# Kernel optimization log

Measured on AMD Instinct MI355X. Metric: run time of the kernel, lower is better.

The kernel has to match this reference:

```python
import jax, jax.numpy as jnp
import numpy as np

N, K, D, P, B = 16384, 64, 128, 8, 32
LN_EPS = 1e-5


def _silu(x):
    return x * jax.nn.sigmoid(x)


def setup_inputs() -> dict:
    key = jax.random.key(0)
    ks = jax.random.split(key, 12)
    s = 1.0 / np.sqrt(D)
    return {
        "x_scalar": jax.random.normal(ks[0], (N, D), jnp.float32),
        "k_dot_r": jax.random.normal(ks[1], (N, K), jnp.float32) * 3.0,
        "sinc_damping": jax.random.uniform(ks[2], (N, K), jnp.float32),
        "batch": jnp.sort(jax.random.randint(ks[3], (N,), 0, B)),
        "down_projection": jax.random.normal(ks[4], (K, P), jnp.float32),
        "W_pre1": jax.random.normal(ks[5], (D, D), jnp.float32) * s,
        "W_pre2": jax.random.normal(ks[6], (D, D), jnp.float32) * s,
        "ln_gamma": jnp.ones((D,), jnp.float32),
        "ln_beta": jnp.zeros((D,), jnp.float32),
        "W_up": jax.random.normal(ks[7], (D, P), jnp.float32) * (1.0 / np.sqrt(P)) * 0.01,
        "W_upd1": jax.random.normal(ks[8], (D, D), jnp.float32) * s,
        "W_upd2": jax.random.normal(ks[9], (D, D), jnp.float32) * s,
    }


def reference(x_scalar, k_dot_r, sinc_damping, batch, down_projection,
              W_pre1, W_pre2, ln_gamma, ln_beta, W_up, W_upd1, W_upd2):
    # pre_mlp residual: x + act(act(x W1^T) W2^T)
    h = _silu(_silu(x_scalar @ W_pre1.T) @ W_pre2.T)
    x_res = x_scalar + h
    # LayerNorm over feature dim
    mu = jnp.mean(x_res, axis=-1, keepdims=True)
    var = jnp.mean(jnp.square(x_res - mu), axis=-1, keepdims=True)
    x_res = (x_res - mu) * jax.lax.rsqrt(var + LN_EPS) * ln_gamma + ln_beta
    # trig structure factors
    real = jnp.cos(k_dot_r) * sinc_damping  # [N, K]
    imag = jnp.sin(k_dot_r) * sinc_damping  # [N, K]
    # scatter-sum per graph: sf[b,k,d] = sum_{n in b} trig[n,k] * x_res[n,d]
    sf_real = jax.ops.segment_sum(real[:, :, None] * x_res[:, None, :], batch, num_segments=B)
    sf_imag = jax.ops.segment_sum(imag[:, :, None] * x_res[:, None, :], batch, num_segments=B)
    # k-space filter: [K, D]
    kfilter = down_projection @ W_up.T
    # gather back per node and reduce over K
    fr = (kfilter[None, :, :] * sf_real)[batch]  # [N, K, D]
    fi = (kfilter[None, :, :] * sf_imag)[batch]  # [N, K, D]
    ewald_message = jnp.einsum('nkd,nk->nd', fr, real) + jnp.einsum('nkd,nk->nd', fi, imag)
    x = x_scalar + ewald_message
    return x + _silu(_silu(x @ W_upd1.T) @ W_upd2.T)
```

## Files before the change

### kernel.cpp

```cpp
#include <hip/hip_runtime.h>
#include <stdint.h>

#define NN 16384
#define KK 64
#define DD 128
#define PP 8
#define NB 32
#define CH 64
#define CHD 32

typedef unsigned short ushort_t;
typedef __attribute__((ext_vector_type(8))) short short8;
typedef __attribute__((ext_vector_type(4))) float f32x4;

__device__ __forceinline__ ushort_t f2bf(float x) {
    unsigned u = __float_as_uint(x);
    u += 0x7fffu + ((u >> 16) & 1u);
    return (ushort_t)(u >> 16);
}
__device__ __forceinline__ float silu_f(float v) { return v / (1.0f + __expf(-v)); }

__device__ __forceinline__ short8 ldWf(const float* __restrict__ W, int row, int col) {
    float4 a = *(const float4*)&W[(size_t)row * DD + col];
    float4 b = *(const float4*)&W[(size_t)row * DD + col + 4];
    short8 v;
    v[0] = (short)f2bf(a.x); v[1] = (short)f2bf(a.y);
    v[2] = (short)f2bf(a.z); v[3] = (short)f2bf(a.w);
    v[4] = (short)f2bf(b.x); v[5] = (short)f2bf(b.y);
    v[6] = (short)f2bf(b.z); v[7] = (short)f2bf(b.w);
    return v;
}

__global__ __launch_bounds__(256, 4) void kB_pre(
        const float* __restrict__ x, const float* __restrict__ W1,
        const float* __restrict__ W2, const float* __restrict__ W3,
        const float* __restrict__ W4, const float* __restrict__ gamma,
        const float* __restrict__ beta, const float* __restrict__ kdr,
        const float* __restrict__ damp, ushort_t* __restrict__ Wb,
        ushort_t* __restrict__ trig_rm, ushort_t* __restrict__ trigTb,
        ushort_t* __restrict__ xresTb) {
    __shared__ __align__(16) ushort_t xsb[32][136];
    __shared__ __align__(16) ushort_t t1b[32][136];
    __shared__ float2 lnp[32][2];
    const int bid = blockIdx.x;

    if (bid < 8) {
        int w = bid;
        const float* s = ((w >> 2) == 0 ? W3 : W4) + (w & 3) * 4096;
        ushort_t* d = Wb + (size_t)(w >> 2) * 16384 + (w & 3) * 4096;
        for (int i = threadIdx.x; i < 4096; i += 256) d[i] = f2bf(s[i]);
        return;
    }

    const int t = threadIdx.x, lane = t & 63, wv = t >> 6;
    const int ci = bid - 8;
    const int n0 = ci * 32;

    float2 kvp[4], dvp[4];
#pragma unroll
    for (int q = 0; q < 4; ++q) {
        int i = t + q * 256;
        int r = i >> 5, kk = (i & 31) * 2;
        kvp[q] = *(const float2*)&kdr[(size_t)(n0 + r) * KK + kk];
        dvp[q] = *(const float2*)&damp[(size_t)(n0 + r) * KK + kk];
    }
    {
        const float4* src = (const float4*)(x + (size_t)n0 * DD);
        for (int i = t; i < 512; i += 256) {
            float4 v0 = src[i * 2], v1 = src[i * 2 + 1];
            int r = i >> 4, c = (i & 15) << 3;
            short8 pk;
            pk[0] = (short)f2bf(v0.x); pk[1] = (short)f2bf(v0.y);
            pk[2] = (short)f2bf(v0.z); pk[3] = (short)f2bf(v0.w);
            pk[4] = (short)f2bf(v1.x); pk[5] = (short)f2bf(v1.y);
            pk[6] = (short)f2bf(v1.z); pk[7] = (short)f2bf(v1.w);
            *(short8*)&xsb[r][c] = pk;
        }
    }
    __syncthreads();

    const int ar0 = (wv & 1) * 16;
    const int chf = (wv >> 1) * 64;
    const int fr = (lane >> 4) * 8, cr = lane & 15, rr4 = (lane >> 4) * 4;
    f32x4 acc[4];
    const f32x4 z4 = {0.f, 0.f, 0.f, 0.f};

#pragma unroll
    for (int nt = 0; nt < 4; ++nt) acc[nt] = z4;
#pragma unroll
    for (int ks = 0; ks < 4; ++ks) {
        short8 af = *(const short8*)&xsb[ar0 + cr][ks * 32 + fr];
#pragma unroll
        for (int nt = 0; nt < 4; ++nt) {
            short8 bf = ldWf(W1, chf + nt * 16 + cr, ks * 32 + fr);
            acc[nt] = __builtin_amdgcn_mfma_f32_16x16x32_bf16(af, bf, acc[nt], 0, 0, 0);
        }
    }
#pragma unroll
    for (int nt = 0; nt < 4; ++nt)
#pragma unroll
        for (int r = 0; r < 4; ++r)
            t1b[ar0 + rr4 + r][chf + nt * 16 + cr] = f2bf(silu_f(acc[nt][r]));
    __syncthreads();

#pragma unroll
    for (int nt = 0; nt < 4; ++nt) acc[nt] = z4;
#pragma unroll
    for (int ks = 0; ks < 4; ++ks) {
        short8 af = *(const short8*)&t1b[ar0 + cr][ks * 32 + fr];
#pragma unroll
        for (int nt = 0; nt < 4; ++nt) {
            short8 bf = ldWf(W2, chf + nt * 16 + cr, ks * 32 + fr);
            acc[nt] = __builtin_amdgcn_mfma_f32_16x16x32_bf16(af, bf, acc[nt], 0, 0, 0);
        }
    }
#pragma unroll
    for (int q = 0; q < 4; ++q) {
        int i = t + q * 256;
        int r = i >> 5, kk = (i & 31) * 2;
        float s0, c0, s1, c1;
        __sincosf(kvp[q].x, &s0, &c0);
        __sincosf(kvp[q].y, &s1, &c1);
        ushort_t rc0 = f2bf(c0 * dvp[q].x), rc1 = f2bf(c1 * dvp[q].y);
        ushort_t is0 = f2bf(s0 * dvp[q].x), is1 = f2bf(s1 * dvp[q].y);
        xsb[r][kk] = rc0; xsb[r][kk + 1] = rc1;
        xsb[r][64 + kk] = is0; xsb[r][64 + kk + 1] = is1;
        ushort2 a; a.x = rc0; a.y = rc1;
        ushort2 b; b.x = is0; b.y = is1;
        *(ushort2*)&trig_rm[(size_t)(n0 + r) * 128 + kk] = a;
        *(ushort2*)&trig_rm[(size_t)(n0 + r) * 128 + 64 + kk] = b;
    }
    float g[4], be[4];
#pragma unroll
    for (int nt = 0; nt < 4; ++nt) {
        g[nt] = gamma[chf + nt * 16 + cr];
        be[nt] = beta[chf + nt * 16 + cr];
    }
#pragma unroll
    for (int r = 0; r < 4; ++r) {
        int row = n0 + ar0 + rr4 + r;
        float s = 0.f, sq = 0.f;
#pragma unroll
        for (int nt = 0; nt < 4; ++nt) {
            float v = x[(size_t)row * DD + chf + nt * 16 + cr] + silu_f(acc[nt][r]);
            acc[nt][r] = v;
            s += v; sq += v * v;
        }
#pragma unroll
        for (int off = 1; off < 16; off <<= 1) {
            s += __shfl_xor(s, off);
            sq += __shfl_xor(sq, off);
        }
        if (cr == 0) {
            float2 p; p.x = s; p.y = sq;
            lnp[ar0 + rr4 + r][wv >> 1] = p;
        }
    }
    __syncthreads();

#pragma unroll
    for (int r = 0; r < 4; ++r) {
        int row = ar0 + rr4 + r;
        float2 a = lnp[row][0], b = lnp[row][1];
        float s = a.x + b.x, sq = a.y + b.y;
        float mu = s * (1.0f / 128.0f);
        float var = sq * (1.0f / 128.0f) - mu * mu;
        float rs = rsqrtf(var + 1e-5f);
#pragma unroll
        for (int nt = 0; nt < 4; ++nt)
            t1b[row][chf + nt * 16 + cr] = f2bf((acc[nt][r] - mu) * rs * g[nt] + be[nt]);
    }
    __syncthreads();

    {
        int m = t >> 1, hh = (t & 1) * 16;
        size_t base = (size_t)(ci >> 1) * 8192 + (size_t)m * 64 + (ci & 1) * 32 + hh;
#pragma unroll
        for (int q = 0; q < 2; ++q) {
            short8 v;
#pragma unroll
            for (int j = 0; j < 8; ++j) v[j] = (short)xsb[hh + q * 8 + j][m];
            *(short8*)&trigTb[base + q * 8] = v;
        }
#pragma unroll
        for (int q = 0; q < 2; ++q) {
            short8 v;
#pragma unroll
            for (int j = 0; j < 8; ++j) v[j] = (short)t1b[hh + q * 8 + j][m];
            *(short8*)&xresTb[base + q * 8] = v;
        }
    }
}

__global__ __launch_bounds__(256, 4) void kS_scatter(
        const int* __restrict__ batch,
        const ushort_t* __restrict__ xresTb, const ushort_t* __restrict__ trigTb,
        const float* __restrict__ dp, const float* __restrict__ wup,
        ushort_t* __restrict__ SFTb) {
    __shared__ __align__(16) ushort_t xt[16][72];
    __shared__ __align__(16) ushort_t tt[64][72];
    __shared__ int seg2[2];
    const int b = blockIdx.x & 31, g2 = blockIdx.x >> 5;
    const int d0 = (g2 & 7) * 16, mh = (g2 >> 3) * 64;
    const int t = threadIdx.x, lane = t & 63, wv = t >> 6;

    if (t < 2) {
        int tgt = b + t;
        int lo = 0, hi = NN;
        while (lo < hi) { int mid = (lo + hi) >> 1; if (batch[mid] < tgt) lo = mid + 1; else hi = mid; }
        seg2[t] = lo;
    }
    __syncthreads();
    const int segs = seg2[0], sege = seg2[1];

    const int fr = (lane >> 4) * 8, cr = lane & 15, rr4 = (lane >> 4) * 4;
    const f32x4 z4 = {0.f, 0.f, 0.f, 0.f};
    f32x4 acc = z4;

    for (int r0 = segs & ~(CH - 1); r0 < sege; r0 += CH) {
        int lo = segs - r0; if (lo < 0) lo = 0;
        int hi = sege - r0; if (hi > CH) hi = CH;
        const size_t cb = (size_t)(r0 >> 6) * 8192;
        for (int i = t; i < 160; i += 256) {
            int row = i >> 1, h = (i & 1) * 32;
            const ushort_t* src = (row < 16 ? xresTb + cb + (size_t)(d0 + row) * 64
                                            : trigTb + cb + (size_t)(mh + row - 16) * 64) + h;
            ushort_t* dst = (row < 16 ? &xt[row][h] : &tt[row - 16][h]);
            if (lo == 0 && hi == CH) {
#pragma unroll
                for (int q = 0; q < 4; ++q) *(short8*)(dst + q * 8) = *(const short8*)(src + q * 8);
            } else {
                for (int j = 0; j < 32; ++j) { int c = h + j; dst[j] = (c >= lo && c < hi) ? src[j] : (ushort_t)0; }
            }
        }
        __syncthreads();
#pragma unroll
        for (int ks = 0; ks < 2; ++ks) {
            short8 af = *(const short8*)&xt[cr][ks * 32 + fr];
            short8 bf = *(const short8*)&tt[wv * 16 + cr][ks * 32 + fr];
            acc = __builtin_amdgcn_mfma_f32_16x16x32_bf16(af, bf, acc, 0, 0, 0);
        }
        __syncthreads();
    }

    const int m = mh + wv * 16 + cr;
    const int k = m & 63;
    float4 p0 = *(const float4*)&dp[k * PP];
    float4 p1 = *(const float4*)&dp[k * PP + 4];
#pragma unroll
    for (int r = 0; r < 4; ++r) {
        int d = d0 + rr4 + r;
        float4 w0 = *(const float4*)&wup[d * PP];
        float4 w1 = *(const float4*)&wup[d * PP + 4];
        float kf = p0.x * w0.x + p0.y * w0.y + p0.z * w0.z + p0.w * w0.w
                 + p1.x * w1.x + p1.y * w1.y + p1.z * w1.z + p1.w * w1.w;
        SFTb[((size_t)b * 128 + d) * 128 + m] = f2bf(acc[r] * kf);
    }
}

__global__ __launch_bounds__(256, 3) void kD_post(
        const float* __restrict__ x, const int* __restrict__ batch,
        const ushort_t* __restrict__ trig_rm, const ushort_t* __restrict__ SFTb,
        const ushort_t* __restrict__ Wb, float* __restrict__ out) {
    __shared__ __align__(16) ushort_t sft[128 * 136];
    __shared__ __align__(16) ushort_t xs[32][136];
    __shared__ int starts[NB + 1];
    __shared__ int offs[NB + 1];
    const int t = threadIdx.x, lane = t & 63, wv = t >> 6;
    const int fr = (lane >> 4) * 8, cr = lane & 15, rr4 = (lane >> 4) * 4;
    const f32x4 z4 = {0.f, 0.f, 0.f, 0.f};

    if (t < 33) {
        int lo;
        if (t == NB) lo = NN;
        else {
            lo = 0; int hi = NN;
            while (lo < hi) { int mid = (lo + hi) >> 1; if (batch[mid] < t) lo = mid + 1; else hi = mid; }
        }
        starts[t] = lo;
    }
    __syncthreads();
    if (t == 0) {
        int off = 0;
        for (int b = 0; b < NB; ++b) {
            offs[b] = off;
            off += (starts[b + 1] - starts[b] + CHD - 1) / CHD;
        }
        offs[NB] = off;
    }
    __syncthreads();
    const int nwl = offs[NB];
    const int c = (blockIdx.x & 7) * 72 + (blockIdx.x >> 3);
    if (c >= nwl) return;
    int b = 0;
    while (offs[b + 1] <= c) ++b;
    const int r0c = starts[b] + (c - offs[b]) * CHD;
    const int len = min(CHD, starts[b + 1] - r0c);

    const int ar0 = (wv & 1) * 16;
    const int chf = (wv >> 1) * 64;
    const ushort_t* W3b = Wb;
    const ushort_t* W4b = Wb + 16384;

    int nrow = r0c + ar0 + cr; if (nrow >= NN) nrow = NN - 1;
    short8 afp[4];
#pragma unroll
    for (int ks = 0; ks < 4; ++ks)
        afp[ks] = *(const short8*)&trig_rm[(size_t)nrow * 128 + ks * 32 + fr];
    float xr[4][4];
#pragma unroll
    for (int nt = 0; nt < 4; ++nt)
#pragma unroll
        for (int r = 0; r < 4; ++r) {
            int row = r0c + ar0 + rr4 + r; if (row >= NN) row = NN - 1;
            xr[nt][r] = x[(size_t)row * DD + chf + nt * 16 + cr];
        }

    {
        const ushort_t* srcS = SFTb + (size_t)b * 16384;
        for (int i = t; i < 2048; i += 256) {
            int r = i >> 4, cc = (i & 15) * 8;
            *(short8*)&sft[r * 136 + cc] = *(const short8*)(srcS + r * 128 + cc);
        }
    }
    __syncthreads();

    f32x4 g4[4];
#pragma unroll
    for (int nt = 0; nt < 4; ++nt) g4[nt] = z4;
#pragma unroll
    for (int ks = 0; ks < 4; ++ks) {
#pragma unroll
        for (int nt = 0; nt < 4; ++nt) {
            short8 bf = *(const short8*)&sft[(chf + nt * 16 + cr) * 136 + ks * 32 + fr];
            g4[nt] = __builtin_amdgcn_mfma_f32_16x16x32_bf16(afp[ks], bf, g4[nt], 0, 0, 0);
        }
    }

    float xk[4][4];
#pragma unroll
    for (int nt = 0; nt < 4; ++nt)
#pragma unroll
        for (int r = 0; r < 4; ++r) {
            int rr = ar0 + rr4 + r;
            float xv = xr[nt][r] + g4[nt][r];
            xk[nt][r] = xv;
            xs[rr][chf + nt * 16 + cr] = f2bf(xv);
        }
    __syncthreads();

#pragma unroll
    for (int nt = 0; nt < 4; ++nt) g4[nt] = z4;
#pragma unroll
    for (int ks = 0; ks < 4; ++ks) {
        short8 af = *(const short8*)&xs[ar0 + cr][ks * 32 + fr];
#pragma unroll
        for (int nt = 0; nt < 4; ++nt) {
            short8 bf = *(const short8*)&W3b[(size_t)(chf + nt * 16 + cr) * DD + ks * 32 + fr];
            g4[nt] = __builtin_amdgcn_mfma_f32_16x16x32_bf16(af, bf, g4[nt], 0, 0, 0);
        }
    }
#pragma unroll
    for (int nt = 0; nt < 4; ++nt)
#pragma unroll
        for (int r = 0; r < 4; ++r)
            sft[(ar0 + rr4 + r) * 136 + chf + nt * 16 + cr] = f2bf(silu_f(g4[nt][r]));
    __syncthreads();

#pragma unroll
    for (int nt = 0; nt < 4; ++nt) g4[nt] = z4;
#pragma unroll
    for (int ks = 0; ks < 4; ++ks) {
        short8 af = *(const short8*)&sft[(ar0 + cr) * 136 + ks * 32 + fr];
#pragma unroll
        for (int nt = 0; nt < 4; ++nt) {
            short8 bf = *(const short8*)&W4b[(size_t)(chf + nt * 16 + cr) * DD + ks * 32 + fr];
            g4[nt] = __builtin_amdgcn_mfma_f32_16x16x32_bf16(af, bf, g4[nt], 0, 0, 0);
        }
    }
#pragma unroll
    for (int nt = 0; nt < 4; ++nt)
#pragma unroll
        for (int r = 0; r < 4; ++r) {
            int rr = ar0 + rr4 + r;
            if (rr < len)
                out[(size_t)(r0c + rr) * DD + chf + nt * 16 + cr] = xk[nt][r] + silu_f(g4[nt][r]);
        }
}

extern "C" void kernel_launch(void* const* d_in, const int* in_sizes, int n_in,
                              void* d_out, int out_size, void* d_ws, size_t ws_size,
                              hipStream_t stream) {
    const float* x      = (const float*)d_in[0];
    const float* kdr    = (const float*)d_in[1];
    const float* damp   = (const float*)d_in[2];
    const int*   batch  = (const int*)d_in[3];
    const float* dp     = (const float*)d_in[4];
    const float* W_pre1 = (const float*)d_in[5];
    const float* W_pre2 = (const float*)d_in[6];
    const float* gamma  = (const float*)d_in[7];
    const float* beta   = (const float*)d_in[8];
    const float* W_up   = (const float*)d_in[9];
    const float* W_upd1 = (const float*)d_in[10];
    const float* W_upd2 = (const float*)d_in[11];
    float* out = (float*)d_out;

    char* w = (char*)d_ws;
    ushort_t* Wb      = (ushort_t*)w;
    size_t o = 131072;
    ushort_t* trig_rm = (ushort_t*)(w + o);  o += (size_t)NN * 128 * 2;
    ushort_t* trigTb  = (ushort_t*)(w + o);  o += (size_t)NN * 128 * 2;
    ushort_t* xresTb  = (ushort_t*)(w + o);  o += (size_t)NN * 128 * 2;
    ushort_t* SFTb    = (ushort_t*)(w + o);  o += (size_t)NB * 128 * 128 * 2;

    hipLaunchKernelGGL(kB_pre, dim3(8 + NN / 32), dim3(256), 0, stream,
                       x, W_pre1, W_pre2, W_upd1, W_upd2, gamma, beta,
                       kdr, damp, Wb, trig_rm, trigTb, xresTb);
    hipLaunchKernelGGL(kS_scatter, dim3(NB * 16), dim3(256), 0, stream,
                       batch, xresTb, trigTb, dp, W_up, SFTb);
    hipLaunchKernelGGL(kD_post, dim3(576), dim3(256), 0, stream,
                       x, batch, trig_rm, SFTb, Wb, out);
}
```

Before: 67.91 us.

## Halve pre-kernel row tile to 16 and compute segment starts once

The pre-MLP/LayerNorm kernel now handles 16 rows per block instead of 32, so it launches twice as many blocks. Each wave covers a 32-column slice, and the LayerNorm partial sums are reduced over four waves. A dedicated block computes the graph segment starts by binary search once and writes them to workspace, so the scatter and post kernels no longer repeat that search in every block. The cost is that W1/W2 fragments are reloaded from global memory twice as often across blocks, and the transposed output writes become narrower.

```diff
diff --git a/kernel.cpp b/kernel.cpp
--- a/kernel.cpp
+++ b/kernel.cpp
@@ -36,12 +36,13 @@
         const float* __restrict__ W2, const float* __restrict__ W3,
         const float* __restrict__ W4, const float* __restrict__ gamma,
         const float* __restrict__ beta, const float* __restrict__ kdr,
-        const float* __restrict__ damp, ushort_t* __restrict__ Wb,
+        const float* __restrict__ damp, const int* __restrict__ batch,
+        ushort_t* __restrict__ Wb, int* __restrict__ starts_g,
         ushort_t* __restrict__ trig_rm, ushort_t* __restrict__ trigTb,
         ushort_t* __restrict__ xresTb) {
-    __shared__ __align__(16) ushort_t xsb[32][136];
-    __shared__ __align__(16) ushort_t t1b[32][136];
-    __shared__ float2 lnp[32][2];
+    __shared__ __align__(16) ushort_t xsb[16][136];
+    __shared__ __align__(16) ushort_t t1b[16][136];
+    __shared__ float2 lnp[16][4];
     const int bid = blockIdx.x;
 
     if (bid < 8) {
@@ -51,14 +52,27 @@
         for (int i = threadIdx.x; i < 4096; i += 256) d[i] = f2bf(s[i]);
         return;
     }
+    if (bid == 8) {
+        const int t = threadIdx.x;
+        if (t <= NB) {
+            int lo;
+            if (t == NB) lo = NN;
+            else {
+                lo = 0; int hi = NN;
+                while (lo < hi) { int mid = (lo + hi) >> 1; if (batch[mid] < t) lo = mid + 1; else hi = mid; }
+            }
+            starts_g[t] = lo;
+        }
+        return;
+    }
 
     const int t = threadIdx.x, lane = t & 63, wv = t >> 6;
-    const int ci = bid - 8;
-    const int n0 = ci * 32;
-
-    float2 kvp[4], dvp[4];
-#pragma unroll
-    for (int q = 0; q < 4; ++q) {
+    const int ci = bid - 9;
+    const int n0 = ci * 16;
+
+    float2 kvp[2], dvp[2];
+#pragma unroll
+    for (int q = 0; q < 2; ++q) {
         int i = t + q * 256;
         int r = i >> 5, kk = (i & 31) * 2;
         kvp[q] = *(const float2*)&kdr[(size_t)(n0 + r) * KK + kk];
@@ -66,56 +80,53 @@
     }
     {
         const float4* src = (const float4*)(x + (size_t)n0 * DD);
-        for (int i = t; i < 512; i += 256) {
-            float4 v0 = src[i * 2], v1 = src[i * 2 + 1];
-            int r = i >> 4, c = (i & 15) << 3;
-            short8 pk;
-            pk[0] = (short)f2bf(v0.x); pk[1] = (short)f2bf(v0.y);
-            pk[2] = (short)f2bf(v0.z); pk[3] = (short)f2bf(v0.w);
-            pk[4] = (short)f2bf(v1.x); pk[5] = (short)f2bf(v1.y);
-            pk[6] = (short)f2bf(v1.z); pk[7] = (short)f2bf(v1.w);
-            *(short8*)&xsb[r][c] = pk;
-        }
-    }
-    __syncthreads();
-
-    const int ar0 = (wv & 1) * 16;
-    const int chf = (wv >> 1) * 64;
+        float4 v0 = src[t * 2], v1 = src[t * 2 + 1];
+        int r = t >> 4, c = (t & 15) << 3;
+        short8 pk;
+        pk[0] = (short)f2bf(v0.x); pk[1] = (short)f2bf(v0.y);
+        pk[2] = (short)f2bf(v0.z); pk[3] = (short)f2bf(v0.w);
+        pk[4] = (short)f2bf(v1.x); pk[5] = (short)f2bf(v1.y);
+        pk[6] = (short)f2bf(v1.z); pk[7] = (short)f2bf(v1.w);
+        *(short8*)&xsb[r][c] = pk;
+    }
+    __syncthreads();
+
+    const int chf = wv * 32;
     const int fr = (lane >> 4) * 8, cr = lane & 15, rr4 = (lane >> 4) * 4;
-    f32x4 acc[4];
+    f32x4 acc[2];
     const f32x4 z4 = {0.f, 0.f, 0.f, 0.f};
 
 #pragma unroll
-    for (int nt = 0; nt < 4; ++nt) acc[nt] = z4;
+    for (int nt = 0; nt < 2; ++nt) acc[nt] = z4;
 #pragma unroll
     for (int ks = 0; ks < 4; ++ks) {
-        short8 af = *(const short8*)&xsb[ar0 + cr][ks * 32 + fr];
-#pragma unroll
-        for (int nt = 0; nt < 4; ++nt) {
+        short8 af = *(const short8*)&xsb[cr][ks * 32 + fr];
+#pragma unroll
+        for (int nt = 0; nt < 2; ++nt) {
             short8 bf = ldWf(W1, chf + nt * 16 + cr, ks * 32 + fr);
             acc[nt] = __builtin_amdgcn_mfma_f32_16x16x32_bf16(af, bf, acc[nt], 0, 0, 0);
         }
     }
 #pragma unroll
-    for (int nt = 0; nt < 4; ++nt)
+    for (int nt = 0; nt < 2; ++nt)
 #pragma unroll
         for (int r = 0; r < 4; ++r)
-            t1b[ar0 + rr4 + r][chf + nt * 16 + cr] = f2bf(silu_f(acc[nt][r]));
-    __syncthreads();
-
-#pragma unroll
-    for (int nt = 0; nt < 4; ++nt) acc[nt] = z4;
+            t1b[rr4 + r][chf + nt * 16 + cr] = f2bf(silu_f(acc[nt][r]));
+    __syncthreads();
+
+#pragma unroll
+    for (int nt = 0; nt < 2; ++nt) acc[nt] = z4;
 #pragma unroll
     for (int ks = 0; ks < 4; ++ks) {
-        short8 af = *(const short8*)&t1b[ar0 + cr][ks * 32 + fr];
-#pragma unroll
-        for (int nt = 0; nt < 4; ++nt) {
+        short8 af = *(const short8*)&t1b[cr][ks * 32 + fr];
+#pragma unroll
+        for (int nt = 0; nt < 2; ++nt) {
             short8 bf = ldWf(W2, chf + nt * 16 + cr, ks * 32 + fr);
             acc[nt] = __builtin_amdgcn_mfma_f32_16x16x32_bf16(af, bf, acc[nt], 0, 0, 0);
         }
     }
 #pragma unroll
-    for (int q = 0; q < 4; ++q) {
+    for (int q = 0; q < 2; ++q) {
         int i = t + q * 256;
         int r = i >> 5, kk = (i & 31) * 2;
         float s0, c0, s1, c1;
@@ -130,18 +141,18 @@
         *(ushort2*)&trig_rm[(size_t)(n0 + r) * 128 + kk] = a;
         *(ushort2*)&trig_rm[(size_t)(n0 + r) * 128 + 64 + kk] = b;
     }
-    float g[4], be[4];
-#pragma unroll
-    for (int nt = 0; nt < 4; ++nt) {
+    float g[2], be[2];
+#pragma unroll
+    for (int nt = 0; nt < 2; ++nt) {
         g[nt] = gamma[chf + nt * 16 + cr];
         be[nt] = beta[chf + nt * 16 + cr];
     }
 #pragma unroll
     for (int r = 0; r < 4; ++r) {
-        int row = n0 + ar0 + rr4 + r;
+        int row = n0 + rr4 + r;
         float s = 0.f, sq = 0.f;
 #pragma unroll
-        for (int nt = 0; nt < 4; ++nt) {
+        for (int nt = 0; nt < 2; ++nt) {
             float v = x[(size_t)row * DD + chf + nt * 16 + cr] + silu_f(acc[nt][r]);
             acc[nt][r] = v;
             s += v; sq += v * v;
@@ -153,47 +164,40 @@
         }
         if (cr == 0) {
             float2 p; p.x = s; p.y = sq;
-            lnp[ar0 + rr4 + r][wv >> 1] = p;
+            lnp[rr4 + r][wv] = p;
         }
     }
     __syncthreads();
 
 #pragma unroll
     for (int r = 0; r < 4; ++r) {
-        int row = ar0 + rr4 + r;
-        float2 a = lnp[row][0], b = lnp[row][1];
-        float s = a.x + b.x, sq = a.y + b.y;
+        int row = rr4 + r;
+        float2 a0 = lnp[row][0], a1 = lnp[row][1], a2 = lnp[row][2], a3 = lnp[row][3];
+        float s = a0.x + a1.x + a2.x + a3.x, sq = a0.y + a1.y + a2.y + a3.y;
         float mu = s * (1.0f / 128.0f);
         float var = sq * (1.0f / 128.0f) - mu * mu;
         float rs = rsqrtf(var + 1e-5f);
 #pragma unroll
-        for (int nt = 0; nt < 4; ++nt)
+        for (int nt = 0; nt < 2; ++nt)
             t1b[row][chf + nt * 16 + cr] = f2bf((acc[nt][r] - mu) * rs * g[nt] + be[nt]);
     }
     __syncthreads();
 
     {
-        int m = t >> 1, hh = (t & 1) * 16;
-        size_t base = (size_t)(ci >> 1) * 8192 + (size_t)m * 64 + (ci & 1) * 32 + hh;
-#pragma unroll
-        for (int q = 0; q < 2; ++q) {
-            short8 v;
-#pragma unroll
-            for (int j = 0; j < 8; ++j) v[j] = (short)xsb[hh + q * 8 + j][m];
-            *(short8*)&trigTb[base + q * 8] = v;
-        }
-#pragma unroll
-        for (int q = 0; q < 2; ++q) {
-            short8 v;
-#pragma unroll
-            for (int j = 0; j < 8; ++j) v[j] = (short)t1b[hh + q * 8 + j][m];
-            *(short8*)&xresTb[base + q * 8] = v;
-        }
+        int m = t >> 1, hh = (t & 1) * 8;
+        size_t base = (size_t)(ci >> 2) * 8192 + (size_t)m * 64 + (ci & 3) * 16 + hh;
+        short8 v;
+#pragma unroll
+        for (int j = 0; j < 8; ++j) v[j] = (short)xsb[hh + j][m];
+        *(short8*)&trigTb[base] = v;
+#pragma unroll
+        for (int j = 0; j < 8; ++j) v[j] = (short)t1b[hh + j][m];
+        *(short8*)&xresTb[base] = v;
     }
 }
 
 __global__ __launch_bounds__(256, 4) void kS_scatter(
-        const int* __restrict__ batch,
+        const int* __restrict__ starts_g,
         const ushort_t* __restrict__ xresTb, const ushort_t* __restrict__ trigTb,
         const float* __restrict__ dp, const float* __restrict__ wup,
         ushort_t* __restrict__ SFTb) {
@@ -204,12 +208,7 @@
     const int d0 = (g2 & 7) * 16, mh = (g2 >> 3) * 64;
     const int t = threadIdx.x, lane = t & 63, wv = t >> 6;
 
-    if (t < 2) {
-        int tgt = b + t;
-        int lo = 0, hi = NN;
-        while (lo < hi) { int mid = (lo + hi) >> 1; if (batch[mid] < tgt) lo = mid + 1; else hi = mid; }
-        seg2[t] = lo;
-    }
+    if (t < 2) seg2[t] = starts_g[b + t];
     __syncthreads();
     const int segs = seg2[0], sege = seg2[1];
 
@@ -259,7 +258,7 @@
 }
 
 __global__ __launch_bounds__(256, 3) void kD_post(
-        const float* __restrict__ x, const int* __restrict__ batch,
+        const float* __restrict__ x, const int* __restrict__ starts_g,
         const ushort_t* __restrict__ trig_rm, const ushort_t* __restrict__ SFTb,
         const ushort_t* __restrict__ Wb, float* __restrict__ out) {
     __shared__ __align__(16) ushort_t sft[128 * 136];
@@ -270,15 +269,7 @@
     const int fr = (lane >> 4) * 8, cr = lane & 15, rr4 = (lane >> 4) * 4;
     const f32x4 z4 = {0.f, 0.f, 0.f, 0.f};
 
-    if (t < 33) {
-        int lo;
-        if (t == NB) lo = NN;
-        else {
-            lo = 0; int hi = NN;
-            while (lo < hi) { int mid = (lo + hi) >> 1; if (batch[mid] < t) lo = mid + 1; else hi = mid; }
-        }
-        starts[t] = lo;
-    }
+    if (t < 33) starts[t] = starts_g[t];
     __syncthreads();
     if (t == 0) {
         int off = 0;
@@ -406,18 +397,19 @@
     float* out = (float*)d_out;
 
     char* w = (char*)d_ws;
-    ushort_t* Wb      = (ushort_t*)w;
+    ushort_t* Wb       = (ushort_t*)w;
+    int*      starts_g = (int*)(w + 65536);
     size_t o = 131072;
     ushort_t* trig_rm = (ushort_t*)(w + o);  o += (size_t)NN * 128 * 2;
     ushort_t* trigTb  = (ushort_t*)(w + o);  o += (size_t)NN * 128 * 2;
     ushort_t* xresTb  = (ushort_t*)(w + o);  o += (size_t)NN * 128 * 2;
     ushort_t* SFTb    = (ushort_t*)(w + o);  o += (size_t)NB * 128 * 128 * 2;
 
-    hipLaunchKernelGGL(kB_pre, dim3(8 + NN / 32), dim3(256), 0, stream,
+    hipLaunchKernelGGL(kB_pre, dim3(9 + NN / 16), dim3(256), 0, stream,
                        x, W_pre1, W_pre2, W_upd1, W_upd2, gamma, beta,
-                       kdr, damp, Wb, trig_rm, trigTb, xresTb);
+                       kdr, damp, batch, Wb, starts_g, trig_rm, trigTb, xresTb);
     hipLaunchKernelGGL(kS_scatter, dim3(NB * 16), dim3(256), 0, stream,
-                       batch, xresTb, trigTb, dp, W_up, SFTb);
+                       starts_g, xresTb, trigTb, dp, W_up, SFTb);
     hipLaunchKernelGGL(kD_post, dim3(576), dim3(256), 0, stream,
-                       x, batch, trig_rm, SFTb, Wb, out);
-}
+                       x, starts_g, trig_rm, SFTb, Wb, out);
+}
```

After: 63.17 us. -7.0%, faster.
